# Performance work log

Measured on AMD Instinct MI355X. Metric: run time of the kernel, lower is better.

Reference implementation:

```python
import jax, jax.numpy as jnp
import numpy as np

SEQ_LEN = 128
INPUT_SIZE = 512
HIDDEN_SIZE = 1024
MEAN_DIM = 3
COV_DIM = 6
HEAD_DIM = 128


def setup_inputs() -> dict:
    key = jax.random.key(0)
    ks = jax.random.split(key, 16)
    B, I, H = 256, INPUT_SIZE, HIDDEN_SIZE
    s_i = 1.0 / np.sqrt(H)
    inp = {
        "encoder_outputs": jax.random.normal(ks[0], (B, 64, H), jnp.float32),
        "encoder_hidden": jax.random.normal(ks[1], (1, B, H), jnp.float32),
        # GRU weights (PyTorch layout: gates ordered r,z,n along dim 0)
        "W_ih": jax.random.uniform(ks[2], (3 * H, I), jnp.float32, -s_i, s_i),
        "W_hh": jax.random.uniform(ks[3], (3 * H, H), jnp.float32, -s_i, s_i),
        "b_ih": jax.random.uniform(ks[4], (3 * H,), jnp.float32, -s_i, s_i),
        "b_hh": jax.random.uniform(ks[5], (3 * H,), jnp.float32, -s_i, s_i),
        # out: Linear(H -> I)
        "W_out": jax.random.uniform(ks[6], (I, H), jnp.float32, -s_i, s_i),
        "b_out": jax.random.uniform(ks[7], (I,), jnp.float32, -s_i, s_i),
        # mean head: I -> 128 -> meanDim
        "Wm1": jax.random.uniform(ks[8], (HEAD_DIM, I), jnp.float32, -1/np.sqrt(I), 1/np.sqrt(I)),
        "bm1": jax.random.uniform(ks[9], (HEAD_DIM,), jnp.float32, -1/np.sqrt(I), 1/np.sqrt(I)),
        "Wm2": jax.random.uniform(ks[10], (MEAN_DIM, HEAD_DIM), jnp.float32, -1/np.sqrt(HEAD_DIM), 1/np.sqrt(HEAD_DIM)),
        "bm2": jax.random.uniform(ks[11], (MEAN_DIM,), jnp.float32, -1/np.sqrt(HEAD_DIM), 1/np.sqrt(HEAD_DIM)),
        # cov head: I -> 128 -> covDim
        "Wc1": jax.random.uniform(ks[12], (HEAD_DIM, I), jnp.float32, -1/np.sqrt(I), 1/np.sqrt(I)),
        "bc1": jax.random.uniform(ks[13], (HEAD_DIM,), jnp.float32, -1/np.sqrt(I), 1/np.sqrt(I)),
        "Wc2": jax.random.uniform(ks[14], (COV_DIM, HEAD_DIM), jnp.float32, -1/np.sqrt(HEAD_DIM), 1/np.sqrt(HEAD_DIM)),
        "bc2": jax.random.uniform(ks[15], (COV_DIM,), jnp.float32, -1/np.sqrt(HEAD_DIM), 1/np.sqrt(HEAD_DIM)),
    }
    return inp


def _gru_decode(x0, h0, W_ih, W_hh, b_ih, b_hh, W_out, b_out):
    def step(carry, _):
        x, h = carry
        xr = jax.nn.relu(x)                          # relu(input.float())
        gi = xr @ W_ih.T + b_ih                      # [B, 3H]
        gh = h @ W_hh.T + b_hh                       # [B, 3H]
        ir, iz, inn = jnp.split(gi, 3, axis=-1)
        hr, hz, hn = jnp.split(gh, 3, axis=-1)
        r = jax.nn.sigmoid(ir + hr)
        z = jax.nn.sigmoid(iz + hz)
        n = jnp.tanh(inn + r * hn)
        h_new = (1.0 - z) * n + z * h
        out = h_new @ W_out.T + b_out                # [B, I]
        return (jax.lax.stop_gradient(out), h_new), out

    (_, _), outs = jax.lax.scan(step, (x0, h0), None, length=SEQ_LEN)
    return jnp.transpose(outs, (1, 0, 2))            # [B, S, I]


def reference(encoder_outputs, encoder_hidden, W_ih, W_hh, b_ih, b_hh,
              W_out, b_out, Wm1, bm1, Wm2, bm2, Wc1, bc1, Wc2, bc2):
    B = encoder_outputs.shape[0]
    h0 = encoder_hidden[0]                           # [B, H]
    x0 = jnp.zeros((B, INPUT_SIZE), jnp.float32)     # deterministic init (torch.empty in orig)
    outs = _gru_decode(x0, h0, W_ih, W_hh, b_ih, b_hh, W_out, b_out)
    means = jax.nn.relu(outs @ Wm1.T + bm1) @ Wm2.T + bm2
    covs = jax.nn.relu(outs @ Wc1.T + bc1) @ Wc2.T + bc2
    return means, covs
```

## Files before the change

kernel.cpp:

```cpp
#include <hip/hip_runtime.h>


#define HID 1024
#define INP 512
#define BATCH 256
#define SEQ 128

typedef _Float16 f16x8 __attribute__((ext_vector_type(8)));
typedef float f32x4 __attribute__((ext_vector_type(4)));

__device__ __forceinline__ float fast_sigmoid(float x) {
    return 1.0f / (1.0f + __expf(-x));
}
__device__ __forceinline__ float fast_tanh(float x) {
    return 1.0f - 2.0f / (__expf(2.0f * x) + 1.0f);
}

__global__ void prep_kernel(const float* __restrict__ Wih, const float* __restrict__ Whh,
                            const float* __restrict__ Wout, const float* __restrict__ Wm1,
                            const float* __restrict__ Wc1, const float* __restrict__ ehid,
                            _Float16* __restrict__ WihH, _Float16* __restrict__ WhhH,
                            _Float16* __restrict__ WoutH, _Float16* __restrict__ Wm1H,
                            _Float16* __restrict__ Wc1H,
                            float* __restrict__ h32, _Float16* __restrict__ h16) {
    const size_t N0 = (size_t)3*HID*INP;
    const size_t N1 = N0 + (size_t)3*HID*HID;
    const size_t N2 = N1 + (size_t)INP*HID;
    const size_t N3 = N2 + (size_t)128*INP;
    const size_t N4 = N3 + (size_t)128*INP;
    const size_t N5 = N4 + (size_t)BATCH*HID;
    size_t stride = (size_t)gridDim.x * blockDim.x;
    for (size_t i = (size_t)blockIdx.x * blockDim.x + threadIdx.x; i < N5; i += stride) {
        if (i < N0) WihH[i] = (_Float16)Wih[i];
        else if (i < N1) WhhH[i - N0] = (_Float16)Whh[i - N0];
        else if (i < N2) WoutH[i - N1] = (_Float16)Wout[i - N1];
        else if (i < N3) Wm1H[i - N2] = (_Float16)Wm1[i - N2];
        else if (i < N4) Wc1H[i - N3] = (_Float16)Wc1[i - N3];
        else { size_t j = i - N4; float v = ehid[j]; h32[j] = v; h16[j] = (_Float16)v; }
    }
}

__global__ __launch_bounds__(256) void gates_kernel(
    const _Float16* __restrict__ WihH, const _Float16* __restrict__ WhhH,
    const float* __restrict__ bih, const float* __restrict__ bhh,
    const _Float16* __restrict__ outs,
    const float* __restrict__ h32p, const _Float16* __restrict__ h16p,
    float* __restrict__ h32n, _Float16* __restrict__ h16n,
    int t)
{
    int w = blockIdx.x;
    int xcd = w & 7;
    int s = w >> 3;
    int jj = xcd * 8 + (s >> 2);
    int b4 = s & 3;
    int wave = threadIdx.x >> 6;
    int lane = threadIdx.x & 63;
    int l15 = lane & 15;
    int koff = (lane >> 4) * 8;
    int row = b4 * 64 + wave * 16 + l15;
    int jcol = jj * 16;

    f32x4 ar = {0.f,0.f,0.f,0.f}, az = {0.f,0.f,0.f,0.f};
    f32x4 ai = {0.f,0.f,0.f,0.f}, ah = {0.f,0.f,0.f,0.f};

    const _Float16* wr = WihH + (size_t)(jcol + l15) * INP + koff;
    const _Float16* wz = wr + (size_t)HID * INP;
    const _Float16* wn = wz + (size_t)HID * INP;
    if (t > 0) {
        const _Float16* xp = outs + ((size_t)row * SEQ + (t - 1)) * INP + koff;
        #pragma unroll 4
        for (int kk = 0; kk < INP; kk += 32) {
            f16x8 a = *(const f16x8*)(xp + kk);
            #pragma unroll
            for (int q = 0; q < 8; ++q) a[q] = a[q] > (_Float16)0.f ? a[q] : (_Float16)0.f;
            f16x8 br = *(const f16x8*)(wr + kk);
            f16x8 bz = *(const f16x8*)(wz + kk);
            f16x8 bn = *(const f16x8*)(wn + kk);
            ar = __builtin_amdgcn_mfma_f32_16x16x32_f16(a, br, ar, 0, 0, 0);
            az = __builtin_amdgcn_mfma_f32_16x16x32_f16(a, bz, az, 0, 0, 0);
            ai = __builtin_amdgcn_mfma_f32_16x16x32_f16(a, bn, ai, 0, 0, 0);
        }
    }
    const _Float16* hr = WhhH + (size_t)(jcol + l15) * HID + koff;
    const _Float16* hz = hr + (size_t)HID * HID;
    const _Float16* hn = hz + (size_t)HID * HID;
    const _Float16* hp = h16p + (size_t)row * HID + koff;
    #pragma unroll 4
    for (int kk = 0; kk < HID; kk += 32) {
        f16x8 a = *(const f16x8*)(hp + kk);
        f16x8 br = *(const f16x8*)(hr + kk);
        f16x8 bz = *(const f16x8*)(hz + kk);
        f16x8 bn = *(const f16x8*)(hn + kk);
        ar = __builtin_amdgcn_mfma_f32_16x16x32_f16(a, br, ar, 0, 0, 0);
        az = __builtin_amdgcn_mfma_f32_16x16x32_f16(a, bz, az, 0, 0, 0);
        ah = __builtin_amdgcn_mfma_f32_16x16x32_f16(a, bn, ah, 0, 0, 0);
    }
    int jc = jcol + l15;
    float brr = bih[jc] + bhh[jc];
    float bzz = bih[HID + jc] + bhh[HID + jc];
    float bin = bih[2 * HID + jc];
    float bhn = bhh[2 * HID + jc];
    int crow0 = b4 * 64 + wave * 16 + (lane >> 4) * 4;
    #pragma unroll
    for (int i = 0; i < 4; ++i) {
        int r = crow0 + i;
        float rr = fast_sigmoid(ar[i] + brr);
        float zz = fast_sigmoid(az[i] + bzz);
        float nn = fast_tanh(ai[i] + bin + rr * (ah[i] + bhn));
        float hold = h32p[(size_t)r * HID + jc];
        float hv = (1.0f - zz) * nn + zz * hold;
        h32n[(size_t)r * HID + jc] = hv;
        h16n[(size_t)r * HID + jc] = (_Float16)hv;
    }
}

__global__ __launch_bounds__(256) void outproj_kernel(
    const _Float16* __restrict__ WoutH, const float* __restrict__ bout,
    const _Float16* __restrict__ h16n, _Float16* __restrict__ outs, int t)
{
    int w = blockIdx.x;
    int b8 = w >> 4;
    int c16 = w & 15;
    int wave = threadIdx.x >> 6;
    int lane = threadIdx.x & 63;
    int l15 = lane & 15;
    int koff = (lane >> 4) * 8;
    int row = b8 * 32 + (wave & 1) * 16 + l15;
    int cbase = c16 * 32 + (wave >> 1) * 16;
    f32x4 acc = {0.f,0.f,0.f,0.f};
    const _Float16* ap = h16n + (size_t)row * HID + koff;
    const _Float16* bp = WoutH + (size_t)(cbase + l15) * HID + koff;
    #pragma unroll 4
    for (int kk = 0; kk < HID; kk += 32) {
        f16x8 a = *(const f16x8*)(ap + kk);
        f16x8 b = *(const f16x8*)(bp + kk);
        acc = __builtin_amdgcn_mfma_f32_16x16x32_f16(a, b, acc, 0, 0, 0);
    }
    int c = cbase + l15;
    float bb = bout[c];
    int crow0 = b8 * 32 + (wave & 1) * 16 + (lane >> 4) * 4;
    #pragma unroll
    for (int i = 0; i < 4; ++i) {
        int r = crow0 + i;
        outs[((size_t)r * SEQ + t) * INP + c] = (_Float16)(acc[i] + bb);
    }
}

__global__ __launch_bounds__(256) void heads_kernel(
    const _Float16* __restrict__ outs,
    const _Float16* __restrict__ Wm1H, const float* __restrict__ bm1,
    const float* __restrict__ Wm2, const float* __restrict__ bm2,
    const _Float16* __restrict__ Wc1H, const float* __restrict__ bc1,
    const float* __restrict__ Wc2, const float* __restrict__ bc2,
    float* __restrict__ dout)
{
    __shared__ _Float16 hid[128][136];
    int b = blockIdx.x;
    int wave = threadIdx.x >> 6;
    int lane = threadIdx.x & 63;
    int l15 = lane & 15;
    int koff = (lane >> 4) * 8;
    const size_t rowbase = (size_t)b * 128;
    for (int head = 0; head < 2; ++head) {
        const _Float16* W1 = head ? Wc1H : Wm1H;
        const float* b1 = head ? bc1 : bm1;
        f32x4 acc[2][8];
        #pragma unroll
        for (int rf = 0; rf < 2; ++rf)
            #pragma unroll
            for (int ct = 0; ct < 8; ++ct) acc[rf][ct] = (f32x4){0.f,0.f,0.f,0.f};
        for (int kk = 0; kk < INP; kk += 32) {
            f16x8 a0 = *(const f16x8*)(outs + (rowbase + wave * 32 + l15) * INP + kk + koff);
            f16x8 a1 = *(const f16x8*)(outs + (rowbase + wave * 32 + 16 + l15) * INP + kk + koff);
            #pragma unroll
            for (int ct = 0; ct < 8; ++ct) {
                f16x8 bb = *(const f16x8*)(W1 + (size_t)(ct * 16 + l15) * INP + kk + koff);
                acc[0][ct] = __builtin_amdgcn_mfma_f32_16x16x32_f16(a0, bb, acc[0][ct], 0, 0, 0);
                acc[1][ct] = __builtin_amdgcn_mfma_f32_16x16x32_f16(a1, bb, acc[1][ct], 0, 0, 0);
            }
        }
        #pragma unroll
        for (int rf = 0; rf < 2; ++rf) {
            int rl = wave * 32 + rf * 16 + (lane >> 4) * 4;
            #pragma unroll
            for (int ct = 0; ct < 8; ++ct) {
                int col = ct * 16 + l15;
                float bb1 = b1[col];
                #pragma unroll
                for (int i = 0; i < 4; ++i) {
                    float v = acc[rf][ct][i] + bb1;
                    hid[rl + i][col] = (_Float16)(v > 0.f ? v : 0.f);
                }
            }
        }
        __syncthreads();
        if (threadIdx.x < 128) {
            int srow = threadIdx.x;
            if (head == 0) {
                float a0 = bm2[0], a1 = bm2[1], a2 = bm2[2];
                for (int k = 0; k < 128; ++k) {
                    float hv = (float)hid[srow][k];
                    a0 += hv * Wm2[k];
                    a1 += hv * Wm2[128 + k];
                    a2 += hv * Wm2[256 + k];
                }
                size_t o = ((size_t)b * 128 + srow) * 3;
                dout[o] = a0; dout[o + 1] = a1; dout[o + 2] = a2;
            } else {
                float a[6];
                #pragma unroll
                for (int m = 0; m < 6; ++m) a[m] = bc2[m];
                for (int k = 0; k < 128; ++k) {
                    float hv = (float)hid[srow][k];
                    #pragma unroll
                    for (int m = 0; m < 6; ++m) a[m] += hv * Wc2[m * 128 + k];
                }
                size_t o = (size_t)BATCH * SEQ * 3 + ((size_t)b * 128 + srow) * 6;
                #pragma unroll
                for (int m = 0; m < 6; ++m) dout[o + m] = a[m];
            }
        }
        __syncthreads();
    }
}

extern "C" void kernel_launch(void* const* d_in, const int* in_sizes, int n_in,
                              void* d_out, int out_size, void* d_ws, size_t ws_size,
                              hipStream_t stream) {
    (void)in_sizes; (void)n_in; (void)out_size; (void)ws_size;
    const float* ehid = (const float*)d_in[1];
    const float* Wih  = (const float*)d_in[2];
    const float* Whh  = (const float*)d_in[3];
    const float* bih  = (const float*)d_in[4];
    const float* bhh  = (const float*)d_in[5];
    const float* Wout = (const float*)d_in[6];
    const float* bout = (const float*)d_in[7];
    const float* Wm1  = (const float*)d_in[8];
    const float* bm1  = (const float*)d_in[9];
    const float* Wm2  = (const float*)d_in[10];
    const float* bm2  = (const float*)d_in[11];
    const float* Wc1  = (const float*)d_in[12];
    const float* bc1  = (const float*)d_in[13];
    const float* Wc2  = (const float*)d_in[14];
    const float* bc2  = (const float*)d_in[15];
    float* dout = (float*)d_out;

    char* ws = (char*)d_ws;
    _Float16* WihH  = (_Float16*)(ws);
    _Float16* WhhH  = (_Float16*)(ws + 3145728);
    _Float16* WoutH = (_Float16*)(ws + 9437184);
    _Float16* Wm1H  = (_Float16*)(ws + 10485760);
    _Float16* Wc1H  = (_Float16*)(ws + 10616832);
    float*    h32   = (float*)   (ws + 10747904);
    _Float16* h16   = (_Float16*)(ws + 12845056);
    _Float16* outs  = (_Float16*)(ws + 13893632);

    prep_kernel<<<2048, 256, 0, stream>>>(Wih, Whh, Wout, Wm1, Wc1, ehid,
                                          WihH, WhhH, WoutH, Wm1H, Wc1H, h32, h16);
    for (int t = 0; t < SEQ; ++t) {
        int cur = t & 1, nxt = (t + 1) & 1;
        gates_kernel<<<256, 256, 0, stream>>>(WihH, WhhH, bih, bhh, outs,
                                              h32 + (size_t)cur * BATCH * HID,
                                              h16 + (size_t)cur * BATCH * HID,
                                              h32 + (size_t)nxt * BATCH * HID,
                                              h16 + (size_t)nxt * BATCH * HID, t);
        outproj_kernel<<<128, 256, 0, stream>>>(WoutH, bout,
                                                h16 + (size_t)nxt * BATCH * HID, outs, t);
    }
    heads_kernel<<<256, 256, 0, stream>>>(outs, Wm1H, bm1, Wm2, bm2,
                                          Wc1H, bc1, Wc2, bc2, dout);
}
```

Measured before the change: 4.497 ms.

## Fuse GRU decode into one persistent cooperative kernel with LDS-resident weights

Replaces the 256 per-step kernel launches and the separate prep and heads kernels with a single cooperative persistent kernel that uses a software grid barrier between the gate and output-projection phases. Each workgroup converts and keeps its slice of W_ih and W_hh in LDS for all timesteps, so the recurrent weights are no longer reread from global memory every step. The output projection now splits K across wave pairs and reduces the halves through shared memory. The cost is two atomic grid barriers per step and a large LDS footprint that limits residency to one block per CU.

Measured after the change: 17.35 ms. 286% more time.

```diff
diff --git a/kernel.cpp b/kernel.cpp
--- a/kernel.cpp
+++ b/kernel.cpp
@@ -5,6 +5,10 @@
 #define INP 512
 #define BATCH 256
 #define SEQ 128
+#define NWG 256
+#define NTHR 256
+#define WIH_LD 520
+#define WHH_LD 1032
 
 typedef _Float16 f16x8 __attribute__((ext_vector_type(8)));
 typedef float f32x4 __attribute__((ext_vector_type(4)));
@@ -16,211 +20,252 @@
     return 1.0f - 2.0f / (__expf(2.0f * x) + 1.0f);
 }
 
-__global__ void prep_kernel(const float* __restrict__ Wih, const float* __restrict__ Whh,
-                            const float* __restrict__ Wout, const float* __restrict__ Wm1,
-                            const float* __restrict__ Wc1, const float* __restrict__ ehid,
-                            _Float16* __restrict__ WihH, _Float16* __restrict__ WhhH,
-                            _Float16* __restrict__ WoutH, _Float16* __restrict__ Wm1H,
-                            _Float16* __restrict__ Wc1H,
-                            float* __restrict__ h32, _Float16* __restrict__ h16) {
-    const size_t N0 = (size_t)3*HID*INP;
-    const size_t N1 = N0 + (size_t)3*HID*HID;
-    const size_t N2 = N1 + (size_t)INP*HID;
-    const size_t N3 = N2 + (size_t)128*INP;
-    const size_t N4 = N3 + (size_t)128*INP;
-    const size_t N5 = N4 + (size_t)BATCH*HID;
-    size_t stride = (size_t)gridDim.x * blockDim.x;
-    for (size_t i = (size_t)blockIdx.x * blockDim.x + threadIdx.x; i < N5; i += stride) {
-        if (i < N0) WihH[i] = (_Float16)Wih[i];
-        else if (i < N1) WhhH[i - N0] = (_Float16)Whh[i - N0];
-        else if (i < N2) WoutH[i - N1] = (_Float16)Wout[i - N1];
-        else if (i < N3) Wm1H[i - N2] = (_Float16)Wm1[i - N2];
-        else if (i < N4) Wc1H[i - N3] = (_Float16)Wc1[i - N3];
-        else { size_t j = i - N4; float v = ehid[j]; h32[j] = v; h16[j] = (_Float16)v; }
-    }
-}
-
-__global__ __launch_bounds__(256) void gates_kernel(
-    const _Float16* __restrict__ WihH, const _Float16* __restrict__ WhhH,
-    const float* __restrict__ bih, const float* __restrict__ bhh,
-    const _Float16* __restrict__ outs,
-    const float* __restrict__ h32p, const _Float16* __restrict__ h16p,
-    float* __restrict__ h32n, _Float16* __restrict__ h16n,
-    int t)
-{
-    int w = blockIdx.x;
-    int xcd = w & 7;
-    int s = w >> 3;
-    int jj = xcd * 8 + (s >> 2);
-    int b4 = s & 3;
-    int wave = threadIdx.x >> 6;
-    int lane = threadIdx.x & 63;
-    int l15 = lane & 15;
-    int koff = (lane >> 4) * 8;
-    int row = b4 * 64 + wave * 16 + l15;
-    int jcol = jj * 16;
-
-    f32x4 ar = {0.f,0.f,0.f,0.f}, az = {0.f,0.f,0.f,0.f};
-    f32x4 ai = {0.f,0.f,0.f,0.f}, ah = {0.f,0.f,0.f,0.f};
-
-    const _Float16* wr = WihH + (size_t)(jcol + l15) * INP + koff;
-    const _Float16* wz = wr + (size_t)HID * INP;
-    const _Float16* wn = wz + (size_t)HID * INP;
-    if (t > 0) {
-        const _Float16* xp = outs + ((size_t)row * SEQ + (t - 1)) * INP + koff;
-        #pragma unroll 4
-        for (int kk = 0; kk < INP; kk += 32) {
-            f16x8 a = *(const f16x8*)(xp + kk);
+struct Params {
+    const float *ehid, *Wih, *Whh, *bih, *bhh, *Wout, *bout;
+    const float *Wm1, *bm1, *Wm2, *bm2, *Wc1, *bc1, *Wc2, *bc2;
+    _Float16 *WoutH, *Wm1H, *Wc1H;
+    float *h32; _Float16 *h16; _Float16 *outs;
+    int *bar; float *dout;
+};
+
+__device__ __forceinline__ void gbar(int* bar) {
+    __threadfence();
+    __syncthreads();
+    if (threadIdx.x == 0) {
+        int g = __hip_atomic_load(bar + 1, __ATOMIC_RELAXED, __HIP_MEMORY_SCOPE_AGENT);
+        int a = __hip_atomic_fetch_add(bar, 1, __ATOMIC_ACQ_REL, __HIP_MEMORY_SCOPE_AGENT);
+        if (a == NWG - 1) {
+            __hip_atomic_store(bar, 0, __ATOMIC_RELAXED, __HIP_MEMORY_SCOPE_AGENT);
+            __hip_atomic_fetch_add(bar + 1, 1, __ATOMIC_RELEASE, __HIP_MEMORY_SCOPE_AGENT);
+        } else {
+            while (__hip_atomic_load(bar + 1, __ATOMIC_ACQUIRE, __HIP_MEMORY_SCOPE_AGENT) == g) {
+                __builtin_amdgcn_s_sleep(2);
+            }
+        }
+    }
+    __syncthreads();
+    __threadfence();
+}
+
+__global__ __launch_bounds__(NTHR, 1) void gru_persistent(Params p) {
+    __shared__ __align__(16) char smraw[3 * 16 * WIH_LD * 2 + 3 * 16 * WHH_LD * 2];
+    __shared__ float red[2 * 16 * 16];
+    _Float16* wih_s = (_Float16*)smraw;
+    _Float16* whh_s = (_Float16*)(smraw + 3 * 16 * WIH_LD * 2);
+    _Float16* hid_s = (_Float16*)smraw;
+
+    const int w = blockIdx.x;
+    const int wave = threadIdx.x >> 6;
+    const int lane = threadIdx.x & 63;
+    const int l15 = lane & 15;
+    const int kq = lane >> 4;
+
+    {
+        const int tid = w * NTHR + threadIdx.x;
+        const int nth = NWG * NTHR;
+        for (int i = tid; i < INP * HID / 4; i += nth) {
+            float4 v = ((const float4*)p.Wout)[i];
+            _Float16* d = p.WoutH + i * 4;
+            d[0] = (_Float16)v.x; d[1] = (_Float16)v.y; d[2] = (_Float16)v.z; d[3] = (_Float16)v.w;
+        }
+        for (int i = tid; i < 128 * INP / 4; i += nth) {
+            float4 v = ((const float4*)p.Wm1)[i];
+            _Float16* d = p.Wm1H + i * 4;
+            d[0] = (_Float16)v.x; d[1] = (_Float16)v.y; d[2] = (_Float16)v.z; d[3] = (_Float16)v.w;
+            float4 u = ((const float4*)p.Wc1)[i];
+            _Float16* e = p.Wc1H + i * 4;
+            e[0] = (_Float16)u.x; e[1] = (_Float16)u.y; e[2] = (_Float16)u.z; e[3] = (_Float16)u.w;
+        }
+        for (int i = tid; i < BATCH * HID / 4; i += nth) {
+            float4 v = ((const float4*)p.ehid)[i];
+            ((float4*)p.h32)[i] = v;
+            _Float16* d = p.h16 + i * 4;
+            d[0] = (_Float16)v.x; d[1] = (_Float16)v.y; d[2] = (_Float16)v.z; d[3] = (_Float16)v.w;
+        }
+    }
+
+    const int jj = w >> 2;
+    const int b4 = w & 3;
+    for (int i = threadIdx.x; i < 3 * 16 * (INP / 4); i += NTHR) {
+        int gi = i / (16 * (INP / 4));
+        int rr = (i / (INP / 4)) % 16;
+        int kk = (i % (INP / 4)) * 4;
+        float4 v = *(const float4*)(p.Wih + ((size_t)(gi * HID + jj * 16 + rr)) * INP + kk);
+        _Float16* d = &wih_s[(gi * 16 + rr) * WIH_LD + kk];
+        d[0] = (_Float16)v.x; d[1] = (_Float16)v.y; d[2] = (_Float16)v.z; d[3] = (_Float16)v.w;
+    }
+    for (int i = threadIdx.x; i < 3 * 16 * (HID / 4); i += NTHR) {
+        int gi = i / (16 * (HID / 4));
+        int rr = (i / (HID / 4)) % 16;
+        int kk = (i % (HID / 4)) * 4;
+        float4 v = *(const float4*)(p.Whh + ((size_t)(gi * HID + jj * 16 + rr)) * HID + kk);
+        _Float16* d = &whh_s[(gi * 16 + rr) * WHH_LD + kk];
+        d[0] = (_Float16)v.x; d[1] = (_Float16)v.y; d[2] = (_Float16)v.z; d[3] = (_Float16)v.w;
+    }
+
+    gbar(p.bar);
+
+    const int jc = jj * 16 + l15;
+    const float brr = p.bih[jc] + p.bhh[jc];
+    const float bzz = p.bih[HID + jc] + p.bhh[HID + jc];
+    const float bin = p.bih[2 * HID + jc];
+    const float bhn = p.bhh[2 * HID + jc];
+    const int grow  = b4 * 64 + wave * 16 + l15;
+    const int gcrow = b4 * 64 + wave * 16 + kq * 4;
+
+    const int ort = w >> 4;
+    const int oct = w & 15;
+    const int csub = wave & 1;
+    const int khalf = wave >> 1;
+    const int orow = ort * 16 + l15;
+    const int ocol = oct * 32 + csub * 16 + l15;
+    const float obout = p.bout[ocol];
+
+    for (int t = 0; t < SEQ; ++t) {
+        const int cur = t & 1, nxt = 1 - cur;
+        const float*    h32p = p.h32 + (size_t)cur * BATCH * HID;
+        float*          h32n = p.h32 + (size_t)nxt * BATCH * HID;
+        const _Float16* h16p = p.h16 + (size_t)cur * BATCH * HID;
+        _Float16*       h16n = p.h16 + (size_t)nxt * BATCH * HID;
+
+        f32x4 ar = {0.f,0.f,0.f,0.f}, az = {0.f,0.f,0.f,0.f};
+        f32x4 ai = {0.f,0.f,0.f,0.f}, ah = {0.f,0.f,0.f,0.f};
+        if (t > 0) {
+            const _Float16* xp = p.outs + ((size_t)grow * SEQ + (t - 1)) * INP + kq * 8;
+            #pragma unroll 4
+            for (int kk = 0; kk < INP; kk += 32) {
+                f16x8 a = *(const f16x8*)(xp + kk);
+                #pragma unroll
+                for (int q = 0; q < 8; ++q) a[q] = a[q] > (_Float16)0.f ? a[q] : (_Float16)0.f;
+                f16x8 br = *(const f16x8*)&wih_s[(0 * 16 + l15) * WIH_LD + kk + kq * 8];
+                f16x8 bz = *(const f16x8*)&wih_s[(1 * 16 + l15) * WIH_LD + kk + kq * 8];
+                f16x8 bn = *(const f16x8*)&wih_s[(2 * 16 + l15) * WIH_LD + kk + kq * 8];
+                ar = __builtin_amdgcn_mfma_f32_16x16x32_f16(a, br, ar, 0, 0, 0);
+                az = __builtin_amdgcn_mfma_f32_16x16x32_f16(a, bz, az, 0, 0, 0);
+                ai = __builtin_amdgcn_mfma_f32_16x16x32_f16(a, bn, ai, 0, 0, 0);
+            }
+        }
+        {
+            const _Float16* hp = h16p + (size_t)grow * HID + kq * 8;
+            #pragma unroll 4
+            for (int kk = 0; kk < HID; kk += 32) {
+                f16x8 a = *(const f16x8*)(hp + kk);
+                f16x8 br = *(const f16x8*)&whh_s[(0 * 16 + l15) * WHH_LD + kk + kq * 8];
+                f16x8 bz = *(const f16x8*)&whh_s[(1 * 16 + l15) * WHH_LD + kk + kq * 8];
+                f16x8 bn = *(const f16x8*)&whh_s[(2 * 16 + l15) * WHH_LD + kk + kq * 8];
+                ar = __builtin_amdgcn_mfma_f32_16x16x32_f16(a, br, ar, 0, 0, 0);
+                az = __builtin_amdgcn_mfma_f32_16x16x32_f16(a, bz, az, 0, 0, 0);
+                ah = __builtin_amdgcn_mfma_f32_16x16x32_f16(a, bn, ah, 0, 0, 0);
+            }
+        }
+        #pragma unroll
+        for (int i = 0; i < 4; ++i) {
+            int r = gcrow + i;
+            float rr = fast_sigmoid(ar[i] + brr);
+            float zz = fast_sigmoid(az[i] + bzz);
+            float nn = fast_tanh(ai[i] + bin + rr * (ah[i] + bhn));
+            float hold = h32p[(size_t)r * HID + jc];
+            float hv = (1.0f - zz) * nn + zz * hold;
+            h32n[(size_t)r * HID + jc] = hv;
+            h16n[(size_t)r * HID + jc] = (_Float16)hv;
+        }
+
+        gbar(p.bar);
+
+        {
+            f32x4 acc = {0.f,0.f,0.f,0.f};
+            const _Float16* ap = h16n + (size_t)orow * HID + khalf * 512 + kq * 8;
+            const _Float16* bp = p.WoutH + (size_t)ocol * HID + khalf * 512 + kq * 8;
+            #pragma unroll 4
+            for (int kk = 0; kk < 512; kk += 32) {
+                f16x8 a = *(const f16x8*)(ap + kk);
+                f16x8 b = *(const f16x8*)(bp + kk);
+                acc = __builtin_amdgcn_mfma_f32_16x16x32_f16(a, b, acc, 0, 0, 0);
+            }
+            if (khalf == 1) {
+                #pragma unroll
+                for (int i = 0; i < 4; ++i)
+                    red[(csub * 16 + kq * 4 + i) * 16 + l15] = acc[i];
+            }
+            __syncthreads();
+            if (khalf == 0) {
+                #pragma unroll
+                for (int i = 0; i < 4; ++i) {
+                    float v = acc[i] + red[(csub * 16 + kq * 4 + i) * 16 + l15];
+                    p.outs[((size_t)(ort * 16 + kq * 4 + i) * SEQ + t) * INP + ocol] =
+                        (_Float16)(v + obout);
+                }
+            }
+        }
+
+        gbar(p.bar);
+    }
+
+    {
+        const int b = w;
+        const size_t rowbase = (size_t)b * SEQ;
+        for (int head = 0; head < 2; ++head) {
+            const _Float16* W1 = head ? p.Wc1H : p.Wm1H;
+            const float* b1 = head ? p.bc1 : p.bm1;
+            f32x4 acc[2][8];
             #pragma unroll
-            for (int q = 0; q < 8; ++q) a[q] = a[q] > (_Float16)0.f ? a[q] : (_Float16)0.f;
-            f16x8 br = *(const f16x8*)(wr + kk);
-            f16x8 bz = *(const f16x8*)(wz + kk);
-            f16x8 bn = *(const f16x8*)(wn + kk);
-            ar = __builtin_amdgcn_mfma_f32_16x16x32_f16(a, br, ar, 0, 0, 0);
-            az = __builtin_amdgcn_mfma_f32_16x16x32_f16(a, bz, az, 0, 0, 0);
-            ai = __builtin_amdgcn_mfma_f32_16x16x32_f16(a, bn, ai, 0, 0, 0);
-        }
-    }
-    const _Float16* hr = WhhH + (size_t)(jcol + l15) * HID + koff;
-    const _Float16* hz = hr + (size_t)HID * HID;
-    const _Float16* hn = hz + (size_t)HID * HID;
-    const _Float16* hp = h16p + (size_t)row * HID + koff;
-    #pragma unroll 4
-    for (int kk = 0; kk < HID; kk += 32) {
-        f16x8 a = *(const f16x8*)(hp + kk);
-        f16x8 br = *(const f16x8*)(hr + kk);
-        f16x8 bz = *(const f16x8*)(hz + kk);
-        f16x8 bn = *(const f16x8*)(hn + kk);
-        ar = __builtin_amdgcn_mfma_f32_16x16x32_f16(a, br, ar, 0, 0, 0);
-        az = __builtin_amdgcn_mfma_f32_16x16x32_f16(a, bz, az, 0, 0, 0);
-        ah = __builtin_amdgcn_mfma_f32_16x16x32_f16(a, bn, ah, 0, 0, 0);
-    }
-    int jc = jcol + l15;
-    float brr = bih[jc] + bhh[jc];
-    float bzz = bih[HID + jc] + bhh[HID + jc];
-    float bin = bih[2 * HID + jc];
-    float bhn = bhh[2 * HID + jc];
-    int crow0 = b4 * 64 + wave * 16 + (lane >> 4) * 4;
-    #pragma unroll
-    for (int i = 0; i < 4; ++i) {
-        int r = crow0 + i;
-        float rr = fast_sigmoid(ar[i] + brr);
-        float zz = fast_sigmoid(az[i] + bzz);
-        float nn = fast_tanh(ai[i] + bin + rr * (ah[i] + bhn));
-        float hold = h32p[(size_t)r * HID + jc];
-        float hv = (1.0f - zz) * nn + zz * hold;
-        h32n[(size_t)r * HID + jc] = hv;
-        h16n[(size_t)r * HID + jc] = (_Float16)hv;
-    }
-}
-
-__global__ __launch_bounds__(256) void outproj_kernel(
-    const _Float16* __restrict__ WoutH, const float* __restrict__ bout,
-    const _Float16* __restrict__ h16n, _Float16* __restrict__ outs, int t)
-{
-    int w = blockIdx.x;
-    int b8 = w >> 4;
-    int c16 = w & 15;
-    int wave = threadIdx.x >> 6;
-    int lane = threadIdx.x & 63;
-    int l15 = lane & 15;
-    int koff = (lane >> 4) * 8;
-    int row = b8 * 32 + (wave & 1) * 16 + l15;
-    int cbase = c16 * 32 + (wave >> 1) * 16;
-    f32x4 acc = {0.f,0.f,0.f,0.f};
-    const _Float16* ap = h16n + (size_t)row * HID + koff;
-    const _Float16* bp = WoutH + (size_t)(cbase + l15) * HID + koff;
-    #pragma unroll 4
-    for (int kk = 0; kk < HID; kk += 32) {
-        f16x8 a = *(const f16x8*)(ap + kk);
-        f16x8 b = *(const f16x8*)(bp + kk);
-        acc = __builtin_amdgcn_mfma_f32_16x16x32_f16(a, b, acc, 0, 0, 0);
-    }
-    int c = cbase + l15;
-    float bb = bout[c];
-    int crow0 = b8 * 32 + (wave & 1) * 16 + (lane >> 4) * 4;
-    #pragma unroll
-    for (int i = 0; i < 4; ++i) {
-        int r = crow0 + i;
-        outs[((size_t)r * SEQ + t) * INP + c] = (_Float16)(acc[i] + bb);
-    }
-}
-
-__global__ __launch_bounds__(256) void heads_kernel(
-    const _Float16* __restrict__ outs,
-    const _Float16* __restrict__ Wm1H, const float* __restrict__ bm1,
-    const float* __restrict__ Wm2, const float* __restrict__ bm2,
-    const _Float16* __restrict__ Wc1H, const float* __restrict__ bc1,
-    const float* __restrict__ Wc2, const float* __restrict__ bc2,
-    float* __restrict__ dout)
-{
-    __shared__ _Float16 hid[128][136];
-    int b = blockIdx.x;
-    int wave = threadIdx.x >> 6;
-    int lane = threadIdx.x & 63;
-    int l15 = lane & 15;
-    int koff = (lane >> 4) * 8;
-    const size_t rowbase = (size_t)b * 128;
-    for (int head = 0; head < 2; ++head) {
-        const _Float16* W1 = head ? Wc1H : Wm1H;
-        const float* b1 = head ? bc1 : bm1;
-        f32x4 acc[2][8];
-        #pragma unroll
-        for (int rf = 0; rf < 2; ++rf)
+            for (int rf = 0; rf < 2; ++rf)
+                #pragma unroll
+                for (int ct = 0; ct < 8; ++ct) acc[rf][ct] = (f32x4){0.f,0.f,0.f,0.f};
+            for (int kk = 0; kk < INP; kk += 32) {
+                f16x8 a0 = *(const f16x8*)(p.outs + (rowbase + wave * 32 + l15) * INP + kk + kq * 8);
+                f16x8 a1 = *(const f16x8*)(p.outs + (rowbase + wave * 32 + 16 + l15) * INP + kk + kq * 8);
+                #pragma unroll
+                for (int ct = 0; ct < 8; ++ct) {
+                    f16x8 bb = *(const f16x8*)(W1 + (size_t)(ct * 16 + l15) * INP + kk + kq * 8);
+                    acc[0][ct] = __builtin_amdgcn_mfma_f32_16x16x32_f16(a0, bb, acc[0][ct], 0, 0, 0);
+                    acc[1][ct] = __builtin_amdgcn_mfma_f32_16x16x32_f16(a1, bb, acc[1][ct], 0, 0, 0);
+                }
+            }
+            __syncthreads();
             #pragma unroll
-            for (int ct = 0; ct < 8; ++ct) acc[rf][ct] = (f32x4){0.f,0.f,0.f,0.f};
-        for (int kk = 0; kk < INP; kk += 32) {
-            f16x8 a0 = *(const f16x8*)(outs + (rowbase + wave * 32 + l15) * INP + kk + koff);
-            f16x8 a1 = *(const f16x8*)(outs + (rowbase + wave * 32 + 16 + l15) * INP + kk + koff);
-            #pragma unroll
-            for (int ct = 0; ct < 8; ++ct) {
-                f16x8 bb = *(const f16x8*)(W1 + (size_t)(ct * 16 + l15) * INP + kk + koff);
-                acc[0][ct] = __builtin_amdgcn_mfma_f32_16x16x32_f16(a0, bb, acc[0][ct], 0, 0, 0);
-                acc[1][ct] = __builtin_amdgcn_mfma_f32_16x16x32_f16(a1, bb, acc[1][ct], 0, 0, 0);
-            }
-        }
-        #pragma unroll
-        for (int rf = 0; rf < 2; ++rf) {
-            int rl = wave * 32 + rf * 16 + (lane >> 4) * 4;
-            #pragma unroll
-            for (int ct = 0; ct < 8; ++ct) {
-                int col = ct * 16 + l15;
-                float bb1 = b1[col];
-                #pragma unroll
-                for (int i = 0; i < 4; ++i) {
-                    float v = acc[rf][ct][i] + bb1;
-                    hid[rl + i][col] = (_Float16)(v > 0.f ? v : 0.f);
+            for (int rf = 0; rf < 2; ++rf) {
+                int rl = wave * 32 + rf * 16 + kq * 4;
+                #pragma unroll
+                for (int ct = 0; ct < 8; ++ct) {
+                    int col = ct * 16 + l15;
+                    float bb1 = b1[col];
+                    #pragma unroll
+                    for (int i = 0; i < 4; ++i) {
+                        float v = acc[rf][ct][i] + bb1;
+                        hid_s[(rl + i) * 136 + col] = (_Float16)(v > 0.f ? v : 0.f);
+                    }
                 }
             }
-        }
-        __syncthreads();
-        if (threadIdx.x < 128) {
-            int srow = threadIdx.x;
-            if (head == 0) {
-                float a0 = bm2[0], a1 = bm2[1], a2 = bm2[2];
-                for (int k = 0; k < 128; ++k) {
-                    float hv = (float)hid[srow][k];
-                    a0 += hv * Wm2[k];
-                    a1 += hv * Wm2[128 + k];
-                    a2 += hv * Wm2[256 + k];
+            __syncthreads();
+            if (threadIdx.x < 128) {
+                int srow = threadIdx.x;
+                if (head == 0) {
+                    float a0 = p.bm2[0], a1 = p.bm2[1], a2 = p.bm2[2];
+                    for (int k = 0; k < 128; ++k) {
+                        float hv = (float)hid_s[srow * 136 + k];
+                        a0 += hv * p.Wm2[k];
+                        a1 += hv * p.Wm2[128 + k];
+                        a2 += hv * p.Wm2[256 + k];
+                    }
+                    size_t o = ((size_t)b * 128 + srow) * 3;
+                    p.dout[o] = a0; p.dout[o + 1] = a1; p.dout[o + 2] = a2;
+                } else {
+                    float a[6];
+                    #pragma unroll
+                    for (int m = 0; m < 6; ++m) a[m] = p.bc2[m];
+                    for (int k = 0; k < 128; ++k) {
+                        float hv = (float)hid_s[srow * 136 + k];
+                        #pragma unroll
+                        for (int m = 0; m < 6; ++m) a[m] += hv * p.Wc2[m * 128 + k];
+                    }
+                    size_t o = (size_t)BATCH * SEQ * 3 + ((size_t)b * 128 + srow) * 6;
+                    #pragma unroll
+                    for (int m = 0; m < 6; ++m) p.dout[o + m] = a[m];
                 }
-                size_t o = ((size_t)b * 128 + srow) * 3;
-                dout[o] = a0; dout[o + 1] = a1; dout[o + 2] = a2;
-            } else {
-                float a[6];
-                #pragma unroll
-                for (int m = 0; m < 6; ++m) a[m] = bc2[m];
-                for (int k = 0; k < 128; ++k) {
-                    float hv = (float)hid[srow][k];
-                    #pragma unroll
-                    for (int m = 0; m < 6; ++m) a[m] += hv * Wc2[m * 128 + k];
-                }
-                size_t o = (size_t)BATCH * SEQ * 3 + ((size_t)b * 128 + srow) * 6;
-                #pragma unroll
-                for (int m = 0; m < 6; ++m) dout[o + m] = a[m];
-            }
-        }
-        __syncthreads();
+            }
+            __syncthreads();
+        }
     }
 }
 
@@ -228,45 +273,35 @@
                               void* d_out, int out_size, void* d_ws, size_t ws_size,
                               hipStream_t stream) {
     (void)in_sizes; (void)n_in; (void)out_size; (void)ws_size;
-    const float* ehid = (const float*)d_in[1];
-    const float* Wih  = (const float*)d_in[2];
-    const float* Whh  = (const float*)d_in[3];
-    const float* bih  = (const float*)d_in[4];
-    const float* bhh  = (const float*)d_in[5];
-    const float* Wout = (const float*)d_in[6];
-    const float* bout = (const float*)d_in[7];
-    const float* Wm1  = (const float*)d_in[8];
-    const float* bm1  = (const float*)d_in[9];
-    const float* Wm2  = (const float*)d_in[10];
-    const float* bm2  = (const float*)d_in[11];
-    const float* Wc1  = (const float*)d_in[12];
-    const float* bc1  = (const float*)d_in[13];
-    const float* Wc2  = (const float*)d_in[14];
-    const float* bc2  = (const float*)d_in[15];
-    float* dout = (float*)d_out;
+    Params prm;
+    prm.ehid = (const float*)d_in[1];
+    prm.Wih  = (const float*)d_in[2];
+    prm.Whh  = (const float*)d_in[3];
+    prm.bih  = (const float*)d_in[4];
+    prm.bhh  = (const float*)d_in[5];
+    prm.Wout = (const float*)d_in[6];
+    prm.bout = (const float*)d_in[7];
+    prm.Wm1  = (const float*)d_in[8];
+    prm.bm1  = (const float*)d_in[9];
+    prm.Wm2  = (const float*)d_in[10];
+    prm.bm2  = (const float*)d_in[11];
+    prm.Wc1  = (const float*)d_in[12];
+    prm.bc1  = (const float*)d_in[13];
+    prm.Wc2  = (const float*)d_in[14];
+    prm.bc2  = (const float*)d_in[15];
+    prm.dout = (float*)d_out;
 
     char* ws = (char*)d_ws;
-    _Float16* WihH  = (_Float16*)(ws);
-    _Float16* WhhH  = (_Float16*)(ws + 3145728);
-    _Float16* WoutH = (_Float16*)(ws + 9437184);
-    _Float16* Wm1H  = (_Float16*)(ws + 10485760);
-    _Float16* Wc1H  = (_Float16*)(ws + 10616832);
-    float*    h32   = (float*)   (ws + 10747904);
-    _Float16* h16   = (_Float16*)(ws + 12845056);
-    _Float16* outs  = (_Float16*)(ws + 13893632);
-
-    prep_kernel<<<2048, 256, 0, stream>>>(Wih, Whh, Wout, Wm1, Wc1, ehid,
-                                          WihH, WhhH, WoutH, Wm1H, Wc1H, h32, h16);
-    for (int t = 0; t < SEQ; ++t) {
-        int cur = t & 1, nxt = (t + 1) & 1;
-        gates_kernel<<<256, 256, 0, stream>>>(WihH, WhhH, bih, bhh, outs,
-                                              h32 + (size_t)cur * BATCH * HID,
-                                              h16 + (size_t)cur * BATCH * HID,
-                                              h32 + (size_t)nxt * BATCH * HID,
-                                              h16 + (size_t)nxt * BATCH * HID, t);
-        outproj_kernel<<<128, 256, 0, stream>>>(WoutH, bout,
-                                                h16 + (size_t)nxt * BATCH * HID, outs, t);
-    }
-    heads_kernel<<<256, 256, 0, stream>>>(outs, Wm1H, bm1, Wm2, bm2,
-                                          Wc1H, bc1, Wc2, bc2, dout);
-}
+    prm.bar   = (int*)ws;
+    prm.WoutH = (_Float16*)(ws + 256);
+    prm.Wm1H  = (_Float16*)(ws + 256 + 1048576);
+    prm.Wc1H  = (_Float16*)(ws + 256 + 1179648);
+    prm.h32   = (float*)   (ws + 256 + 1310720);
+    prm.h16   = (_Float16*)(ws + 256 + 3407872);
+    prm.outs  = (_Float16*)(ws + 256 + 4456448);
+
+    hipMemsetAsync(ws, 0, 256, stream);
+    void* args[] = { &prm };
+    hipLaunchCooperativeKernel((void*)gru_persistent, dim3(NWG), dim3(NTHR),
+                               args, 0, stream);
+}
```
